# Optimization experiments

Measured on AMD Instinct MI355X. Metric: run time of the kernel, lower is better.

## Reference

```python
import jax, jax.numpy as jnp
import numpy as np

N_STATE = 5
N_CONTROL = 5
NEURONS = 1024
BATCH = 131072
IN_DIM = 3 * N_STATE + 2 * N_CONTROL  # 25


def setup_inputs() -> dict:
    key = jax.random.key(0)
    ks = jax.random.split(key, 11)

    def w(k, shape, fan_in):
        return jax.random.normal(k, shape, jnp.float32) / np.sqrt(fan_in).astype(np.float32)

    return {
        "x": jax.random.normal(ks[0], (BATCH, IN_DIM), jnp.float32),
        "Wx": w(ks[1], (2, N_STATE), N_STATE),
        "bx": jnp.zeros((2,), jnp.float32),
        "Wu": w(ks[2], (2, N_CONTROL), N_CONTROL),
        "bu": jnp.zeros((2,), jnp.float32),
        "W1": w(ks[3], (NEURONS, 10), 10),
        "b1": jnp.zeros((NEURONS,), jnp.float32),
        "W2": w(ks[4], (NEURONS, NEURONS), NEURONS),
        "b2": jnp.zeros((NEURONS,), jnp.float32),
        "W3": w(ks[5], (3, NEURONS), NEURONS),
        "b3": jnp.zeros((3,), jnp.float32),
    }


def reference(x, Wx, bx, Wu, bu, W1, b1, W2, b2, W3, b3):
    ns = Wx.shape[1]
    # strided gathers over the interleaved state/control layout (vectorized over batch)
    vx_ = x[:, 0:3 * ns:3]          # [B, n_state]
    vy_ = x[:, 1:3 * ns:3]
    r_ = x[:, 2:3 * ns:3]
    th_ = x[:, 3 * ns::2]           # [B, n_control]
    st_ = x[:, 3 * ns + 1::2]

    fx = lambda v: jax.nn.relu(v @ Wx.T + bx)  # [B, 2]
    fu = lambda v: jax.nn.relu(v @ Wu.T + bu)  # [B, 2]

    l1 = jnp.concatenate([fx(vx_), fx(vy_), fx(r_), fu(th_), fu(st_)], axis=-1)  # [B, 10]
    l1 = l1[:, None, :]  # unsqueeze(1) -> [B, 1, 10]

    h = jax.nn.relu(l1 @ W1.T + b1)   # [B, 1, neurons]
    h = jax.nn.relu(h @ W2.T + b2)    # [B, 1, neurons]
    return jax.nn.sigmoid(h @ W3.T + b3)  # [B, 1, 3]
```

## Files before the change

kernel.cpp:

```cpp
#include <hip/hip_runtime.h>
#include <stdint.h>

#define NEUR 1024
#define BM 64
#define THREADS 512
#define H1S 2064

typedef short  s16x8  __attribute__((ext_vector_type(8)));
typedef __bf16 bf16x8 __attribute__((ext_vector_type(8)));
typedef float  f32x16 __attribute__((ext_vector_type(16)));

__device__ __forceinline__ unsigned short f2bf(float f){
  unsigned u = __builtin_bit_cast(unsigned, f);
  u += 0x7FFFu + ((u >> 16) & 1u);
  return (unsigned short)(u >> 16);
}
__device__ __forceinline__ float bf2f(unsigned short h){
  unsigned u = ((unsigned)h) << 16;
  return __builtin_bit_cast(float, u);
}
__device__ __forceinline__ f32x16 mfma32(bf16x8 a, bf16x8 b, f32x16 c){
  return __builtin_amdgcn_mfma_f32_32x32x16_bf16(a, b, c, 0, 0, 0);
}
__device__ __forceinline__ f32x16 zero16(){
  f32x16 v;
#pragma unroll
  for (int r = 0; r < 16; ++r) v[r] = 0.f;
  return v;
}
__device__ __forceinline__ bf16x8 ld16(const void* p){
  return __builtin_bit_cast(bf16x8, *reinterpret_cast<const s16x8*>(p));
}

__global__ void prep_kernel(const float* __restrict__ W1, const float* __restrict__ W2,
                            unsigned short* __restrict__ w2opt, unsigned short* __restrict__ w1opt){
  const int nchunks = NEUR * 128;
  const int total = nchunks + 4096;
  for (int i = blockIdx.x*blockDim.x + threadIdx.x; i < total; i += gridDim.x*blockDim.x){
    if (i < nchunks){
      const int col = i >> 7, c8 = i & 127;
      const float* src = W2 + (size_t)col*NEUR + c8*8;
      const int ks = c8 >> 1, lf = c8 & 1, lane = lf*32 + (col & 31), nt = col >> 5;
      unsigned short* dst = w2opt + (((size_t)(nt*64 + ks)*64 + lane) * 8);
#pragma unroll
      for (int j = 0; j < 8; ++j) dst[j] = f2bf(src[j]);
    } else {
      const int o = i - nchunks;
      const int nt = o >> 7, ks = (o >> 6) & 1, lane = o & 63;
      const int col = nt*32 + (lane & 31);
      unsigned short* dst = w1opt + (size_t)o * 8;
#pragma unroll
      for (int j = 0; j < 8; ++j){
        const int k = ks*16 + (lane >> 5)*8 + j;
        dst[j] = (k < 10) ? f2bf(W1[col*10 + k]) : (unsigned short)0;
      }
    }
  }
}

template<bool BFWS>
__global__ __launch_bounds__(THREADS, 2) void mlp_kernel(
    const float* __restrict__ x,
    const float* __restrict__ Wx, const float* __restrict__ bxp,
    const float* __restrict__ Wu, const float* __restrict__ bup,
    const float* __restrict__ W1, const float* __restrict__ b1,
    const float* __restrict__ W2f, const float* __restrict__ b2,
    const float* __restrict__ W3, const float* __restrict__ b3,
    const unsigned short* __restrict__ w2opt, const unsigned short* __restrict__ w1opt,
    float* __restrict__ out)
{
  extern __shared__ char smem[];
  unsigned short* l1p = (unsigned short*)smem;
  char* h1            = smem + 5120;

  const int tid = threadIdx.x;
  const int l   = tid & 63;
  const int wid = tid >> 6;
  const int l31 = l & 31;
  const int lh  = l >> 5;
  const long rbase = (long)blockIdx.x * BM;

  float* xs = (float*)h1;
  for (int i = tid; i < BM*25; i += THREADS) xs[i] = x[rbase*25 + i];
  __syncthreads();

  if (tid < BM){
    const float* xr = xs + tid*25;
    float l1v[10];
#pragma unroll
    for (int g = 0; g < 3; ++g)
#pragma unroll
      for (int o = 0; o < 2; ++o){
        float s = bxp[o];
#pragma unroll
        for (int i = 0; i < 5; ++i) s += xr[g + 3*i] * Wx[o*5 + i];
        l1v[g*2 + o] = fmaxf(s, 0.f);
      }
#pragma unroll
    for (int g = 0; g < 2; ++g)
#pragma unroll
      for (int o = 0; o < 2; ++o){
        float s = bup[o];
#pragma unroll
        for (int i = 0; i < 5; ++i) s += xr[15 + g + 2*i] * Wu[o*5 + i];
        l1v[6 + g*2 + o] = fmaxf(s, 0.f);
      }
    unsigned short* dst = l1p + tid*40;
#pragma unroll
    for (int i = 0; i < 10; ++i) dst[i] = f2bf(l1v[i]);
#pragma unroll
    for (int i = 10; i < 32; ++i) dst[i] = 0;
  }
  __syncthreads();

  {
    f32x16 c[2][4];
#pragma unroll
    for (int mt = 0; mt < 2; ++mt)
#pragma unroll
      for (int nt = 0; nt < 4; ++nt) c[mt][nt] = zero16();

#pragma unroll
    for (int ks = 0; ks < 2; ++ks){
      bf16x8 a0 = ld16(smem + l31*80 + ks*32 + lh*16);
      bf16x8 a1 = ld16(smem + (32 + l31)*80 + ks*32 + lh*16);
      bf16x8 b[4];
#pragma unroll
      for (int nt = 0; nt < 4; ++nt){
        if constexpr (BFWS){
          b[nt] = ld16(w1opt + (((size_t)((wid*4 + nt)*2 + ks)*64 + l) * 8));
        } else {
          const int col = wid*128 + nt*32 + l31;
          s16x8 raw;
#pragma unroll
          for (int j = 0; j < 8; ++j){
            const int k = ks*16 + lh*8 + j;
            raw[j] = (k < 10) ? (short)f2bf(W1[col*10 + k]) : (short)0;
          }
          b[nt] = __builtin_bit_cast(bf16x8, raw);
        }
      }
#pragma unroll
      for (int nt = 0; nt < 4; ++nt){
        c[0][nt] = mfma32(a0, b[nt], c[0][nt]);
        c[1][nt] = mfma32(a1, b[nt], c[1][nt]);
      }
    }
#pragma unroll
    for (int nt = 0; nt < 4; ++nt){
      const int col = wid*128 + nt*32 + l31;
      const float bv = b1[col];
#pragma unroll
      for (int mt = 0; mt < 2; ++mt)
#pragma unroll
        for (int r = 0; r < 16; ++r){
          const int row = mt*32 + (r & 3) + 8*(r >> 2) + 4*lh;
          *reinterpret_cast<unsigned short*>(h1 + row*H1S + col*2) =
              f2bf(fmaxf(c[mt][nt][r] + bv, 0.f));
        }
    }
  }
  __syncthreads();

  f32x16 acc[2][4];
#pragma unroll
  for (int mt = 0; mt < 2; ++mt)
#pragma unroll
    for (int nt = 0; nt < 4; ++nt) acc[mt][nt] = zero16();

  if constexpr (BFWS){
    const char* pb0 = (const char*)(w2opt + ((size_t)(wid*4 + 0)*4096 + l) * 8);
    const char* pb1 = (const char*)(w2opt + ((size_t)(wid*4 + 1)*4096 + l) * 8);
    const char* pb2 = (const char*)(w2opt + ((size_t)(wid*4 + 2)*4096 + l) * 8);
    const char* pb3 = (const char*)(w2opt + ((size_t)(wid*4 + 3)*4096 + l) * 8);
    int ao = l31*H1S + lh*16;

    bf16x8 Aa0, Aa1, Ab0, Ab1;
    bf16x8 P0a, P0b;
    bf16x8 Q0a, Q0b;
    bf16x8 P1a, P1b;
    bf16x8 Q1a, Q1b;

#define MM4_01(A0_,A1_,B0_,B1_) do{ __builtin_amdgcn_s_setprio(1);            \
      acc[0][0]=mfma32(A0_,B0_,acc[0][0]); acc[1][0]=mfma32(A1_,B0_,acc[1][0]);\
      acc[0][1]=mfma32(A0_,B1_,acc[0][1]); acc[1][1]=mfma32(A1_,B1_,acc[1][1]);\
      __builtin_amdgcn_s_setprio(0); }while(0)
#define MM4_23(A0_,A1_,B0_,B1_) do{ __builtin_amdgcn_s_setprio(1);            \
      acc[0][2]=mfma32(A0_,B0_,acc[0][2]); acc[1][2]=mfma32(A1_,B0_,acc[1][2]);\
      acc[0][3]=mfma32(A0_,B1_,acc[0][3]); acc[1][3]=mfma32(A1_,B1_,acc[1][3]);\
      __builtin_amdgcn_s_setprio(0); }while(0)

    P0a = ld16(pb0);          P0b = ld16(pb1);
    Q0a = ld16(pb2);          Q0b = ld16(pb3);
    P1a = ld16(pb0 + 1024);   P1b = ld16(pb1 + 1024);
    Aa0 = ld16(h1 + ao);      Aa1 = ld16(h1 + ao + 32*H1S);

    for (int t = 0; t < 31; ++t){
      Q1a = ld16(pb2 + 1024);  Q1b = ld16(pb3 + 1024);
      Ab0 = ld16(h1 + ao + 32); Ab1 = ld16(h1 + ao + 32*H1S + 32);
      MM4_01(Aa0, Aa1, P0a, P0b);
      P0a = ld16(pb0 + 2048);  P0b = ld16(pb1 + 2048);
      MM4_23(Aa0, Aa1, Q0a, Q0b);
      Q0a = ld16(pb2 + 2048);  Q0b = ld16(pb3 + 2048);
      Aa0 = ld16(h1 + ao + 64); Aa1 = ld16(h1 + ao + 32*H1S + 64);
      MM4_01(Ab0, Ab1, P1a, P1b);
      P1a = ld16(pb0 + 3072);  P1b = ld16(pb1 + 3072);
      MM4_23(Ab0, Ab1, Q1a, Q1b);
      pb0 += 2048; pb1 += 2048; pb2 += 2048; pb3 += 2048; ao += 64;
    }
    Q1a = ld16(pb2 + 1024);  Q1b = ld16(pb3 + 1024);
    Ab0 = ld16(h1 + ao + 32); Ab1 = ld16(h1 + ao + 32*H1S + 32);
    MM4_01(Aa0, Aa1, P0a, P0b);
    MM4_23(Aa0, Aa1, Q0a, Q0b);
    MM4_01(Ab0, Ab1, P1a, P1b);
    MM4_23(Ab0, Ab1, Q1a, Q1b);
#undef MM4_01
#undef MM4_23
  } else {
    const int aA0 = l31*H1S + lh*16;
    for (int ks = 0; ks < 64; ++ks){
      bf16x8 A0 = ld16(h1 + aA0 + ks*32);
      bf16x8 A1 = ld16(h1 + aA0 + 32*H1S + ks*32);
      bf16x8 B[4];
#pragma unroll
      for (int nt = 0; nt < 4; ++nt){
        const int col = wid*128 + nt*32 + l31;
        const float* p = W2f + (size_t)col*NEUR + ks*16 + lh*8;
        s16x8 raw;
#pragma unroll
        for (int j = 0; j < 8; ++j) raw[j] = (short)f2bf(p[j]);
        B[nt] = __builtin_bit_cast(bf16x8, raw);
      }
#pragma unroll
      for (int nt = 0; nt < 4; ++nt){
        acc[0][nt] = mfma32(A0, B[nt], acc[0][nt]);
        acc[1][nt] = mfma32(A1, B[nt], acc[1][nt]);
      }
    }
  }
  __syncthreads();

#pragma unroll
  for (int nt = 0; nt < 4; ++nt){
    const int col = wid*128 + nt*32 + l31;
    const float bv = b2[col];
#pragma unroll
    for (int mt = 0; mt < 2; ++mt)
#pragma unroll
      for (int r = 0; r < 16; ++r){
        const int row = mt*32 + (r & 3) + 8*(r >> 2) + 4*lh;
        *reinterpret_cast<unsigned short*>(h1 + row*H1S + col*2) =
            f2bf(fmaxf(acc[mt][nt][r] + bv, 0.f));
      }
  }
  __syncthreads();

  float s[8][3];
#pragma unroll
  for (int rr = 0; rr < 8; ++rr)
#pragma unroll
    for (int j = 0; j < 3; ++j) s[rr][j] = 0.f;

#pragma unroll
  for (int h = 0; h < 2; ++h){
    const int k0 = h*512 + l*8;
    float w3v[3][8];
#pragma unroll
    for (int j = 0; j < 3; ++j)
#pragma unroll
      for (int i = 0; i < 8; ++i) w3v[j][i] = W3[j*NEUR + k0 + i];
#pragma unroll
    for (int rr = 0; rr < 8; ++rr){
      const int row = wid*8 + rr;
      s16x8 raw = *reinterpret_cast<const s16x8*>(h1 + row*H1S + k0*2);
#pragma unroll
      for (int i = 0; i < 8; ++i){
        const float hv = bf2f((unsigned short)raw[i]);
        s[rr][0] += hv * w3v[0][i];
        s[rr][1] += hv * w3v[1][i];
        s[rr][2] += hv * w3v[2][i];
      }
    }
  }
#pragma unroll
  for (int off = 1; off < 64; off <<= 1)
#pragma unroll
    for (int rr = 0; rr < 8; ++rr)
#pragma unroll
      for (int j = 0; j < 3; ++j) s[rr][j] += __shfl_xor(s[rr][j], off, 64);

  if (l == 0){
#pragma unroll
    for (int rr = 0; rr < 8; ++rr){
      const int row = wid*8 + rr;
#pragma unroll
      for (int j = 0; j < 3; ++j)
        out[(rbase + row)*3 + j] = 1.f / (1.f + __expf(-(s[rr][j] + b3[j])));
    }
  }
}

extern "C" void kernel_launch(void* const* d_in, const int* in_sizes, int n_in,
                              void* d_out, int out_size, void* d_ws, size_t ws_size,
                              hipStream_t stream){
  const float* x  = (const float*)d_in[0];
  const float* Wx = (const float*)d_in[1];
  const float* bx = (const float*)d_in[2];
  const float* Wu = (const float*)d_in[3];
  const float* bu = (const float*)d_in[4];
  const float* W1 = (const float*)d_in[5];
  const float* b1 = (const float*)d_in[6];
  const float* W2 = (const float*)d_in[7];
  const float* b2 = (const float*)d_in[8];
  const float* W3 = (const float*)d_in[9];
  const float* b3 = (const float*)d_in[10];
  float* out = (float*)d_out;

  const int batch   = in_sizes[0] / 25;
  const int nblocks = batch / BM;
  const size_t ws_need = (size_t)(32*64*64*8 + 4096*8) * sizeof(unsigned short);
  const int smem = 5120 + BM*H1S;

  if (ws_size >= ws_need){
    unsigned short* w2opt = (unsigned short*)d_ws;
    unsigned short* w1opt = w2opt + (size_t)32*64*64*8;
    prep_kernel<<<512, 256, 0, stream>>>(W1, W2, w2opt, w1opt);
    hipFuncSetAttribute(reinterpret_cast<const void*>(mlp_kernel<true>),
                        hipFuncAttributeMaxDynamicSharedMemorySize, smem);
    mlp_kernel<true><<<nblocks, THREADS, smem, stream>>>(
        x, Wx, bx, Wu, bu, W1, b1, W2, b2, W3, b3, w2opt, w1opt, out);
  } else {
    hipFuncSetAttribute(reinterpret_cast<const void*>(mlp_kernel<false>),
                        hipFuncAttributeMaxDynamicSharedMemorySize, smem);
    mlp_kernel<false><<<nblocks, THREADS, smem, stream>>>(
        x, Wx, bx, Wu, bu, W1, b1, W2, b2, W3, b3, nullptr, nullptr, out);
  }
}
```

Measured before the change: 309.8 us.

## Split layer-2 output columns across block pairs with 128-row tiles and K-halved h1

Each block now processes 128 batch rows and half (512) of the layer-2 output neurons. Layer-1 activations are produced in two K-halves of 512 columns so the shared buffer shrinks. Layer 3 is fused into the layer-2 epilogue from registers via shuffles, and the two column-half partial sums are written to workspace and combined by a new finish kernel that applies the sigmoid. This targets better reuse of W2 per block and avoids the layer-2 activation round-trip through LDS. The cost is that layer-1 is recomputed by both blocks of a pair, and there is an extra kernel launch plus a workspace round trip.

```diff
diff --git a/kernel.cpp b/kernel.cpp
--- a/kernel.cpp
+++ b/kernel.cpp
@@ -2,9 +2,11 @@
 #include <stdint.h>
 
 #define NEUR 1024
-#define BM 64
+#define BM 128
+#define BN 512
 #define THREADS 512
-#define H1S 2064
+#define H1S 1040
+#define L1S 80
 
 typedef short  s16x8  __attribute__((ext_vector_type(8)));
 typedef __bf16 bf16x8 __attribute__((ext_vector_type(8)));
@@ -58,27 +60,39 @@
   }
 }
 
-template<bool BFWS>
+__global__ void finish_kernel(const float* __restrict__ pws, const float* __restrict__ b3,
+                              float* __restrict__ out, int batch){
+  const int total = batch * 3;
+  for (int i = blockIdx.x*blockDim.x + threadIdx.x; i < total; i += gridDim.x*blockDim.x){
+    const int j = i - (i/3)*3;
+    const float v = pws[i] + pws[(size_t)total + i] + b3[j];
+    out[i] = 1.f / (1.f + __expf(-v));
+  }
+}
+
 __global__ __launch_bounds__(THREADS, 2) void mlp_kernel(
     const float* __restrict__ x,
     const float* __restrict__ Wx, const float* __restrict__ bxp,
     const float* __restrict__ Wu, const float* __restrict__ bup,
-    const float* __restrict__ W1, const float* __restrict__ b1,
-    const float* __restrict__ W2f, const float* __restrict__ b2,
-    const float* __restrict__ W3, const float* __restrict__ b3,
+    const float* __restrict__ b1, const float* __restrict__ b2,
+    const float* __restrict__ W3,
     const unsigned short* __restrict__ w2opt, const unsigned short* __restrict__ w1opt,
-    float* __restrict__ out)
+    float* __restrict__ pws, int batch)
 {
   extern __shared__ char smem[];
-  unsigned short* l1p = (unsigned short*)smem;
-  char* h1            = smem + 5120;
+  char* l1p = smem;
+  char* h1  = smem + BM*L1S;
 
   const int tid = threadIdx.x;
   const int l   = tid & 63;
   const int wid = tid >> 6;
   const int l31 = l & 31;
   const int lh  = l >> 5;
-  const long rbase = (long)blockIdx.x * BM;
+  const int wm  = wid >> 2;
+  const int wn  = wid & 3;
+  const int bm  = blockIdx.x >> 1;
+  const int bn  = blockIdx.x & 1;
+  const long rbase = (long)bm * BM;
 
   float* xs = (float*)h1;
   for (int i = tid; i < BM*25; i += THREADS) xs[i] = x[rbase*25 + i];
@@ -105,7 +119,7 @@
         for (int i = 0; i < 5; ++i) s += xr[15 + g + 2*i] * Wu[o*5 + i];
         l1v[6 + g*2 + o] = fmaxf(s, 0.f);
       }
-    unsigned short* dst = l1p + tid*40;
+    unsigned short* dst = (unsigned short*)(l1p + tid*L1S);
 #pragma unroll
     for (int i = 0; i < 10; ++i) dst[i] = f2bf(l1v[i]);
 #pragma unroll
@@ -113,73 +127,59 @@
   }
   __syncthreads();
 
-  {
-    f32x16 c[2][4];
-#pragma unroll
-    for (int mt = 0; mt < 2; ++mt)
-#pragma unroll
-      for (int nt = 0; nt < 4; ++nt) c[mt][nt] = zero16();
-
-#pragma unroll
-    for (int ks = 0; ks < 2; ++ks){
-      bf16x8 a0 = ld16(smem + l31*80 + ks*32 + lh*16);
-      bf16x8 a1 = ld16(smem + (32 + l31)*80 + ks*32 + lh*16);
-      bf16x8 b[4];
-#pragma unroll
-      for (int nt = 0; nt < 4; ++nt){
-        if constexpr (BFWS){
-          b[nt] = ld16(w1opt + (((size_t)((wid*4 + nt)*2 + ks)*64 + l) * 8));
-        } else {
-          const int col = wid*128 + nt*32 + l31;
-          s16x8 raw;
-#pragma unroll
-          for (int j = 0; j < 8; ++j){
-            const int k = ks*16 + lh*8 + j;
-            raw[j] = (k < 10) ? (short)f2bf(W1[col*10 + k]) : (short)0;
-          }
-          b[nt] = __builtin_bit_cast(bf16x8, raw);
+  f32x16 acc[2][4];
+#pragma unroll
+  for (int mt = 0; mt < 2; ++mt)
+#pragma unroll
+    for (int nt = 0; nt < 4; ++nt) acc[mt][nt] = zero16();
+
+  const int aBase = (wm*64 + l31)*H1S + lh*16;
+
+  for (int h = 0; h < 2; ++h){
+#pragma unroll
+    for (int st = 0; st < 2; ++st){
+      f32x16 c00 = zero16(), c01 = zero16(), c10 = zero16(), c11 = zero16();
+      const int colh = st*256 + wn*64;
+      const int ntg  = h*16 + st*8 + wn*2;
+#pragma unroll
+      for (int ks = 0; ks < 2; ++ks){
+        bf16x8 a0 = ld16(l1p + (wm*64 + l31)*L1S + ks*32 + lh*16);
+        bf16x8 a1 = ld16(l1p + (wm*64 + 32 + l31)*L1S + ks*32 + lh*16);
+        bf16x8 b0 = ld16(w1opt + (((size_t)(ntg + 0)*2 + ks)*64 + l) * 8);
+        bf16x8 b1f= ld16(w1opt + (((size_t)(ntg + 1)*2 + ks)*64 + l) * 8);
+        c00 = mfma32(a0, b0, c00);
+        c10 = mfma32(a1, b0, c10);
+        c01 = mfma32(a0, b1f, c01);
+        c11 = mfma32(a1, b1f, c11);
+      }
+#pragma unroll
+      for (int nt2 = 0; nt2 < 2; ++nt2){
+        const int colHalf = colh + nt2*32 + l31;
+        const float bv = b1[h*512 + colHalf];
+        const f32x16& cA = nt2 ? c01 : c00;
+        const f32x16& cB = nt2 ? c11 : c10;
+#pragma unroll
+        for (int r = 0; r < 16; ++r){
+          const int rr = (r & 3) + 8*(r >> 2) + 4*lh;
+          *reinterpret_cast<unsigned short*>(h1 + (wm*64 + rr)*H1S + colHalf*2) =
+              f2bf(fmaxf(cA[r] + bv, 0.f));
+          *reinterpret_cast<unsigned short*>(h1 + (wm*64 + 32 + rr)*H1S + colHalf*2) =
+              f2bf(fmaxf(cB[r] + bv, 0.f));
         }
       }
-#pragma unroll
-      for (int nt = 0; nt < 4; ++nt){
-        c[0][nt] = mfma32(a0, b[nt], c[0][nt]);
-        c[1][nt] = mfma32(a1, b[nt], c[1][nt]);
-      }
-    }
-#pragma unroll
-    for (int nt = 0; nt < 4; ++nt){
-      const int col = wid*128 + nt*32 + l31;
-      const float bv = b1[col];
-#pragma unroll
-      for (int mt = 0; mt < 2; ++mt)
-#pragma unroll
-        for (int r = 0; r < 16; ++r){
-          const int row = mt*32 + (r & 3) + 8*(r >> 2) + 4*lh;
-          *reinterpret_cast<unsigned short*>(h1 + row*H1S + col*2) =
-              f2bf(fmaxf(c[mt][nt][r] + bv, 0.f));
-        }
-    }
-  }
-  __syncthreads();
-
-  f32x16 acc[2][4];
-#pragma unroll
-  for (int mt = 0; mt < 2; ++mt)
-#pragma unroll
-    for (int nt = 0; nt < 4; ++nt) acc[mt][nt] = zero16();
-
-  if constexpr (BFWS){
-    const char* pb0 = (const char*)(w2opt + ((size_t)(wid*4 + 0)*4096 + l) * 8);
-    const char* pb1 = (const char*)(w2opt + ((size_t)(wid*4 + 1)*4096 + l) * 8);
-    const char* pb2 = (const char*)(w2opt + ((size_t)(wid*4 + 2)*4096 + l) * 8);
-    const char* pb3 = (const char*)(w2opt + ((size_t)(wid*4 + 3)*4096 + l) * 8);
-    int ao = l31*H1S + lh*16;
-
-    bf16x8 Aa0, Aa1, Ab0, Ab1;
-    bf16x8 P0a, P0b;
-    bf16x8 Q0a, Q0b;
-    bf16x8 P1a, P1b;
-    bf16x8 Q1a, Q1b;
+    }
+    __syncthreads();
+
+    {
+      const size_t hoff = (size_t)h * 32768;
+      const char* pb0 = (const char*)w2opt + (((size_t)(bn*16 + wn*4 + 0)*64)*64 + l)*16 + hoff;
+      const char* pb1 = (const char*)w2opt + (((size_t)(bn*16 + wn*4 + 1)*64)*64 + l)*16 + hoff;
+      const char* pb2 = (const char*)w2opt + (((size_t)(bn*16 + wn*4 + 2)*64)*64 + l)*16 + hoff;
+      const char* pb3 = (const char*)w2opt + (((size_t)(bn*16 + wn*4 + 3)*64)*64 + l)*16 + hoff;
+      int ao = aBase;
+
+      bf16x8 Aa0, Aa1, Ab0, Ab1;
+      bf16x8 P0a, P0b, Q0a, Q0b, P1a, P1b, Q1a, Q1b;
 
 #define MM4_01(A0_,A1_,B0_,B1_) do{ __builtin_amdgcn_s_setprio(1);            \
       acc[0][0]=mfma32(A0_,B0_,acc[0][0]); acc[1][0]=mfma32(A1_,B0_,acc[1][0]);\
@@ -190,56 +190,197 @@
       acc[0][3]=mfma32(A0_,B1_,acc[0][3]); acc[1][3]=mfma32(A1_,B1_,acc[1][3]);\
       __builtin_amdgcn_s_setprio(0); }while(0)
 
-    P0a = ld16(pb0);          P0b = ld16(pb1);
-    Q0a = ld16(pb2);          Q0b = ld16(pb3);
-    P1a = ld16(pb0 + 1024);   P1b = ld16(pb1 + 1024);
-    Aa0 = ld16(h1 + ao);      Aa1 = ld16(h1 + ao + 32*H1S);
-
-    for (int t = 0; t < 31; ++t){
+      P0a = ld16(pb0);          P0b = ld16(pb1);
+      Q0a = ld16(pb2);          Q0b = ld16(pb3);
+      P1a = ld16(pb0 + 1024);   P1b = ld16(pb1 + 1024);
+      Aa0 = ld16(h1 + ao);      Aa1 = ld16(h1 + ao + 32*H1S);
+
+      for (int t = 0; t < 15; ++t){
+        Q1a = ld16(pb2 + 1024);  Q1b = ld16(pb3 + 1024);
+        Ab0 = ld16(h1 + ao + 32); Ab1 = ld16(h1 + ao + 32*H1S + 32);
+        MM4_01(Aa0, Aa1, P0a, P0b);
+        P0a = ld16(pb0 + 2048);  P0b = ld16(pb1 + 2048);
+        MM4_23(Aa0, Aa1, Q0a, Q0b);
+        Q0a = ld16(pb2 + 2048);  Q0b = ld16(pb3 + 2048);
+        Aa0 = ld16(h1 + ao + 64); Aa1 = ld16(h1 + ao + 32*H1S + 64);
+        MM4_01(Ab0, Ab1, P1a, P1b);
+        P1a = ld16(pb0 + 3072);  P1b = ld16(pb1 + 3072);
+        MM4_23(Ab0, Ab1, Q1a, Q1b);
+        pb0 += 2048; pb1 += 2048; pb2 += 2048; pb3 += 2048; ao += 64;
+      }
       Q1a = ld16(pb2 + 1024);  Q1b = ld16(pb3 + 1024);
       Ab0 = ld16(h1 + ao + 32); Ab1 = ld16(h1 + ao + 32*H1S + 32);
       MM4_01(Aa0, Aa1, P0a, P0b);
-      P0a = ld16(pb0 + 2048);  P0b = ld16(pb1 + 2048);
       MM4_23(Aa0, Aa1, Q0a, Q0b);
-      Q0a = ld16(pb2 + 2048);  Q0b = ld16(pb3 + 2048);
-      Aa0 = ld16(h1 + ao + 64); Aa1 = ld16(h1 + ao + 32*H1S + 64);
       MM4_01(Ab0, Ab1, P1a, P1b);
-      P1a = ld16(pb0 + 3072);  P1b = ld16(pb1 + 3072);
       MM4_23(Ab0, Ab1, Q1a, Q1b);
-      pb0 += 2048; pb1 += 2048; pb2 += 2048; pb3 += 2048; ao += 64;
-    }
-    Q1a = ld16(pb2 + 1024);  Q1b = ld16(pb3 + 1024);
-    Ab0 = ld16(h1 + ao + 32); Ab1 = ld16(h1 + ao + 32*H1S + 32);
-    MM4_01(Aa0, Aa1, P0a, P0b);
-    MM4_23(Aa0, Aa1, Q0a, Q0b);
-    MM4_01(Ab0, Ab1, P1a, P1b);
-    MM4_23(Ab0, Ab1, Q1a, Q1b);
 #undef MM4_01
 #undef MM4_23
-  } else {
-    const int aA0 = l31*H1S + lh*16;
-    for (int ks = 0; ks < 64; ++ks){
-      bf16x8 A0 = ld16(h1 + aA0 + ks*32);
-      bf16x8 A1 = ld16(h1 + aA0 + 32*H1S + ks*32);
-      bf16x8 B[4];
-#pragma unroll
-      for (int nt = 0; nt < 4; ++nt){
-        const int col = wid*128 + nt*32 + l31;
-        const float* p = W2f + (size_t)col*NEUR + ks*16 + lh*8;
-        s16x8 raw;
-#pragma unroll
-        for (int j = 0; j < 8; ++j) raw[j] = (short)f2bf(p[j]);
-        B[nt] = __builtin_bit_cast(bf16x8, raw);
-      }
-#pragma unroll
-      for (int nt = 0; nt < 4; ++nt){
-        acc[0][nt] = mfma32(A0, B[nt], acc[0][nt]);
-        acc[1][nt] = mfma32(A1, B[nt], acc[1][nt]);
-      }
-    }
-  }
-  __syncthreads();
-
+    }
+    __syncthreads();
+  }
+
+  float* sp = (float*)l1p;
+  {
+    float b2v[4], w30[4], w31[4], w32[4];
+#pragma unroll
+    for (int nt = 0; nt < 4; ++nt){
+      const int colg = bn*512 + wn*128 + nt*32 + l31;
+      b2v[nt] = b2[colg];
+      w30[nt] = W3[0*NEUR + colg];
+      w31[nt] = W3[1*NEUR + colg];
+      w32[nt] = W3[2*NEUR + colg];
+    }
+#pragma unroll
+    for (int mf = 0; mf < 2; ++mf){
+      float p0[16], p1[16], p2[16];
+#pragma unroll
+      for (int r = 0; r < 16; ++r){ p0[r] = 0.f; p1[r] = 0.f; p2[r] = 0.f; }
+#pragma unroll
+      for (int nt = 0; nt < 4; ++nt)
+#pragma unroll
+        for (int r = 0; r < 16; ++r){
+          const float hv = fmaxf(acc[mf][nt][r] + b2v[nt], 0.f);
+          p0[r] += hv * w30[nt];
+          p1[r] += hv * w31[nt];
+          p2[r] += hv * w32[nt];
+        }
+#pragma unroll
+      for (int off = 1; off < 32; off <<= 1)
+#pragma unroll
+        for (int r = 0; r < 16; ++r){
+          p0[r] += __shfl_xor(p0[r], off, 64);
+          p1[r] += __shfl_xor(p1[r], off, 64);
+          p2[r] += __shfl_xor(p2[r], off, 64);
+        }
+      if (l31 == 0){
+#pragma unroll
+        for (int r = 0; r < 16; ++r){
+          const int row = wm*64 + mf*32 + (r & 3) + 8*(r >> 2) + 4*lh;
+          float* d = sp + ((size_t)wn*BM + row)*3;
+          d[0] = p0[r]; d[1] = p1[r]; d[2] = p2[r];
+        }
+      }
+    }
+  }
+  __syncthreads();
+
+  for (int t2 = tid; t2 < BM*3; t2 += THREADS){
+    const int row = t2 / 3, j = t2 - row*3;
+    const float v = sp[(0*BM + row)*3 + j] + sp[(1*BM + row)*3 + j]
+                  + sp[(2*BM + row)*3 + j] + sp[(3*BM + row)*3 + j];
+    pws[((size_t)bn*batch + rbase + row)*3 + j] = v;
+  }
+}
+
+__global__ __launch_bounds__(THREADS, 2) void mlp_kernel_old(
+    const float* __restrict__ x,
+    const float* __restrict__ Wx, const float* __restrict__ bxp,
+    const float* __restrict__ Wu, const float* __restrict__ bup,
+    const float* __restrict__ W1, const float* __restrict__ b1,
+    const float* __restrict__ W2f, const float* __restrict__ b2,
+    const float* __restrict__ W3, const float* __restrict__ b3,
+    float* __restrict__ out)
+{
+  extern __shared__ char smem[];
+  unsigned short* l1p = (unsigned short*)smem;
+  char* h1 = smem + 5120;
+  const int tid = threadIdx.x, l = tid & 63, wid = tid >> 6;
+  const int l31 = l & 31, lh = l >> 5;
+  const long rbase = (long)blockIdx.x * 64;
+
+  float* xs = (float*)h1;
+  for (int i = tid; i < 64*25; i += THREADS) xs[i] = x[rbase*25 + i];
+  __syncthreads();
+  if (tid < 64){
+    const float* xr = xs + tid*25;
+    float l1v[10];
+#pragma unroll
+    for (int g = 0; g < 3; ++g)
+#pragma unroll
+      for (int o = 0; o < 2; ++o){
+        float s = bxp[o];
+#pragma unroll
+        for (int i = 0; i < 5; ++i) s += xr[g + 3*i] * Wx[o*5 + i];
+        l1v[g*2 + o] = fmaxf(s, 0.f);
+      }
+#pragma unroll
+    for (int g = 0; g < 2; ++g)
+#pragma unroll
+      for (int o = 0; o < 2; ++o){
+        float s = bup[o];
+#pragma unroll
+        for (int i = 0; i < 5; ++i) s += xr[15 + g + 2*i] * Wu[o*5 + i];
+        l1v[6 + g*2 + o] = fmaxf(s, 0.f);
+      }
+    unsigned short* dst = l1p + tid*40;
+#pragma unroll
+    for (int i = 0; i < 10; ++i) dst[i] = f2bf(l1v[i]);
+#pragma unroll
+    for (int i = 10; i < 32; ++i) dst[i] = 0;
+  }
+  __syncthreads();
+
+  f32x16 c[2][4];
+#pragma unroll
+  for (int mt = 0; mt < 2; ++mt)
+#pragma unroll
+    for (int nt = 0; nt < 4; ++nt) c[mt][nt] = zero16();
+#pragma unroll
+  for (int ks = 0; ks < 2; ++ks){
+    bf16x8 a0 = ld16(smem + l31*80 + ks*32 + lh*16);
+    bf16x8 a1 = ld16(smem + (32 + l31)*80 + ks*32 + lh*16);
+#pragma unroll
+    for (int nt = 0; nt < 4; ++nt){
+      const int col = wid*128 + nt*32 + l31;
+      s16x8 raw;
+#pragma unroll
+      for (int j = 0; j < 8; ++j){
+        const int k = ks*16 + lh*8 + j;
+        raw[j] = (k < 10) ? (short)f2bf(W1[col*10 + k]) : (short)0;
+      }
+      bf16x8 b = __builtin_bit_cast(bf16x8, raw);
+      c[0][nt] = mfma32(a0, b, c[0][nt]);
+      c[1][nt] = mfma32(a1, b, c[1][nt]);
+    }
+  }
+#pragma unroll
+  for (int nt = 0; nt < 4; ++nt){
+    const int col = wid*128 + nt*32 + l31;
+    const float bv = b1[col];
+#pragma unroll
+    for (int mt = 0; mt < 2; ++mt)
+#pragma unroll
+      for (int r = 0; r < 16; ++r){
+        const int row = mt*32 + (r & 3) + 8*(r >> 2) + 4*lh;
+        *reinterpret_cast<unsigned short*>(h1 + row*2064 + col*2) =
+            f2bf(fmaxf(c[mt][nt][r] + bv, 0.f));
+      }
+  }
+  __syncthreads();
+
+  f32x16 acc[2][4];
+#pragma unroll
+  for (int mt = 0; mt < 2; ++mt)
+#pragma unroll
+    for (int nt = 0; nt < 4; ++nt) acc[mt][nt] = zero16();
+  const int aA0 = l31*2064 + lh*16;
+  for (int ks = 0; ks < 64; ++ks){
+    bf16x8 A0 = ld16(h1 + aA0 + ks*32);
+    bf16x8 A1 = ld16(h1 + aA0 + 32*2064 + ks*32);
+#pragma unroll
+    for (int nt = 0; nt < 4; ++nt){
+      const int col = wid*128 + nt*32 + l31;
+      const float* p = W2f + (size_t)col*NEUR + ks*16 + lh*8;
+      s16x8 raw;
+#pragma unroll
+      for (int j = 0; j < 8; ++j) raw[j] = (short)f2bf(p[j]);
+      bf16x8 B = __builtin_bit_cast(bf16x8, raw);
+      acc[0][nt] = mfma32(A0, B, acc[0][nt]);
+      acc[1][nt] = mfma32(A1, B, acc[1][nt]);
+    }
+  }
+  __syncthreads();
 #pragma unroll
   for (int nt = 0; nt < 4; ++nt){
     const int col = wid*128 + nt*32 + l31;
@@ -249,18 +390,16 @@
 #pragma unroll
       for (int r = 0; r < 16; ++r){
         const int row = mt*32 + (r & 3) + 8*(r >> 2) + 4*lh;
-        *reinterpret_cast<unsigned short*>(h1 + row*H1S + col*2) =
+        *reinterpret_cast<unsigned short*>(h1 + row*2064 + col*2) =
             f2bf(fmaxf(acc[mt][nt][r] + bv, 0.f));
       }
   }
   __syncthreads();
-
   float s[8][3];
 #pragma unroll
   for (int rr = 0; rr < 8; ++rr)
 #pragma unroll
     for (int j = 0; j < 3; ++j) s[rr][j] = 0.f;
-
 #pragma unroll
   for (int h = 0; h < 2; ++h){
     const int k0 = h*512 + l*8;
@@ -272,7 +411,7 @@
 #pragma unroll
     for (int rr = 0; rr < 8; ++rr){
       const int row = wid*8 + rr;
-      s16x8 raw = *reinterpret_cast<const s16x8*>(h1 + row*H1S + k0*2);
+      s16x8 raw = *reinterpret_cast<const s16x8*>(h1 + row*2064 + k0*2);
 #pragma unroll
       for (int i = 0; i < 8; ++i){
         const float hv = bf2f((unsigned short)raw[i]);
@@ -288,7 +427,6 @@
     for (int rr = 0; rr < 8; ++rr)
 #pragma unroll
       for (int j = 0; j < 3; ++j) s[rr][j] += __shfl_xor(s[rr][j], off, 64);
-
   if (l == 0){
 #pragma unroll
     for (int rr = 0; rr < 8; ++rr){
@@ -316,23 +454,32 @@
   const float* b3 = (const float*)d_in[10];
   float* out = (float*)d_out;
 
-  const int batch   = in_sizes[0] / 25;
-  const int nblocks = batch / BM;
-  const size_t ws_need = (size_t)(32*64*64*8 + 4096*8) * sizeof(unsigned short);
-  const int smem = 5120 + BM*H1S;
-
-  if (ws_size >= ws_need){
+  const int batch = in_sizes[0] / 25;
+  const size_t w2_bytes  = (size_t)NEUR*NEUR*2;
+  const size_t w1_bytes  = (size_t)4096*8*2;
+  const size_t pws_bytes = (size_t)batch*3*2*4;
+  const size_t ws_need   = w2_bytes + w1_bytes + pws_bytes;
+
+  if (ws_size >= ws_need && (batch % BM) == 0){
     unsigned short* w2opt = (unsigned short*)d_ws;
-    unsigned short* w1opt = w2opt + (size_t)32*64*64*8;
+    unsigned short* w1opt = (unsigned short*)((char*)d_ws + w2_bytes);
+    float* pws            = (float*)((char*)d_ws + w2_bytes + w1_bytes);
+
     prep_kernel<<<512, 256, 0, stream>>>(W1, W2, w2opt, w1opt);
-    hipFuncSetAttribute(reinterpret_cast<const void*>(mlp_kernel<true>),
+
+    const int smem = BM*L1S + BM*H1S;
+    hipFuncSetAttribute(reinterpret_cast<const void*>(mlp_kernel),
                         hipFuncAttributeMaxDynamicSharedMemorySize, smem);
-    mlp_kernel<true><<<nblocks, THREADS, smem, stream>>>(
-        x, Wx, bx, Wu, bu, W1, b1, W2, b2, W3, b3, w2opt, w1opt, out);
+    const int nblocks = (batch / BM) * 2;
+    mlp_kernel<<<nblocks, THREADS, smem, stream>>>(
+        x, Wx, bx, Wu, bu, b1, b2, W3, w2opt, w1opt, pws, batch);
+
+    finish_kernel<<<(batch*3 + 255)/256, 256, 0, stream>>>(pws, b3, out, batch);
   } else {
-    hipFuncSetAttribute(reinterpret_cast<const void*>(mlp_kernel<false>),
+    const int smem = 5120 + 64*2064;
+    hipFuncSetAttribute(reinterpret_cast<const void*>(mlp_kernel_old),
                         hipFuncAttributeMaxDynamicSharedMemorySize, smem);
-    mlp_kernel<false><<<nblocks, THREADS, smem, stream>>>(
-        x, Wx, bx, Wu, bu, W1, b1, W2, b2, W3, b3, nullptr, nullptr, out);
-  }
-}
+    mlp_kernel_old<<<batch/64, THREADS, smem, stream>>>(
+        x, Wx, bx, Wu, bu, W1, b1, W2, b2, W3, b3, out);
+  }
+}
```

Result: slower. 363.7 us (+17.4%).
